# Optimization experiments

Hardware: AMD Instinct MI355X
Metric: run time of the kernel (lower is better)

Reference implementation:

```python
import jax, jax.numpy as jnp
import numpy as np

B, S, D = 4, 2048, 1024
H = 3 * D  # MLP hidden


def setup_inputs() -> dict:
    key = jax.random.key(0)
    ks = jax.random.split(key, 12)
    s = 1.0 / np.sqrt(D)
    n = lambda k, shape, sc: (jax.random.normal(k, shape, jnp.float32) * sc)
    return {
        "x": n(ks[0], (B, S, D), 1.0),
        "ln1_g": jnp.ones((D,), jnp.float32), "ln1_b": jnp.zeros((D,), jnp.float32),
        "ln2_g": jnp.ones((D,), jnp.float32), "ln2_b": jnp.zeros((D,), jnp.float32),
        "Wq": n(ks[1], (D, D), s), "bq": jnp.zeros((D,), jnp.float32),
        "Wk": n(ks[2], (D, D), s), "bk": jnp.zeros((D,), jnp.float32),
        "Wv": n(ks[3], (D, D), s), "bv": jnp.zeros((D,), jnp.float32),
        "Wi": n(ks[4], (D, 1), s), "bi": jnp.zeros((1,), jnp.float32),
        "Wf": n(ks[5], (D, 1), s), "bf": jnp.zeros((1,), jnp.float32),
        "Wo": n(ks[6], (D, D), s), "bo": jnp.zeros((D,), jnp.float32),
        "W1": n(ks[7], (D, H), s), "b1": jnp.zeros((H,), jnp.float32),
        "W2": n(ks[8], (H, D), 1.0 / np.sqrt(H)), "b2": jnp.zeros((D,), jnp.float32),
    }


def _layernorm(x, g, b, eps=1e-5):
    m = jnp.mean(x, axis=-1, keepdims=True)
    v = jnp.mean(jnp.square(x - m), axis=-1, keepdims=True)
    return (x - m) * jax.lax.rsqrt(v + eps) * g + b


def reference(x, ln1_g, ln1_b, ln2_g, ln2_b, Wq, bq, Wk, bk, Wv, bv,
              Wi, bi, Wf, bf, Wo, bo, W1, b1, W2, b2):
    seq = x.shape[1]
    h = _layernorm(x, ln1_g, ln1_b)
    # q, k computed in the original but unused in the score matrix (kept faithful)
    q = h @ Wq + bq
    k = h @ Wk + bk
    v = h @ Wv + bv                                  # [B,S,D]
    log_f = jax.nn.log_sigmoid(h @ Wf + bf)          # [B,S,1]
    log_i = jax.nn.log_sigmoid(h @ Wi + bi)          # [B,S,1]
    o = jax.nn.sigmoid(h @ Wo + bo)                  # [B,S,D]
    log_f_cum = jnp.cumsum(log_f, axis=1)            # [B,S,1]
    # log_scores[b,t,s] = log_i[b,s] + log_f_cum[b,t] - log_f_cum[b,s]
    log_scores = jnp.swapaxes(log_i, 1, 2) + log_f_cum - jnp.swapaxes(log_f_cum, 1, 2)
    causal = jnp.triu(jnp.full((seq, seq), -1e9, jnp.float32), k=1)
    scores = jnp.exp(log_scores + causal[None])      # [B,S,S]
    scores = scores / (jnp.sum(scores, axis=-1, keepdims=True) + 1e-6)
    attn = scores @ v                                # [B,S,D]
    x = x + o * attn
    h2 = _layernorm(x, ln2_g, ln2_b)
    m = h2 @ W1 + b1
    m = jnp.square(jnp.where(m > 0, m, 0.01 * m))    # LeakyReLU then square
    x = x + m @ W2 + b2
    return x
```

## Files before the change

kernel.cpp:

```cpp
#include <hip/hip_runtime.h>
#include <hip/hip_bf16.h>
#include <cstdint>

#define DI __device__ __forceinline__
typedef unsigned short u16;
using f32x4 = __attribute__((ext_vector_type(4))) float;
using bf16x8 = __attribute__((ext_vector_type(8))) short;

DI float bf16_bits_to_f32(u16 h) { return __uint_as_float(((unsigned int)h) << 16); }
DI u16 f32_to_bf16_bits(float f) {
    unsigned int u = __float_as_uint(f);
    unsigned int lsb = (u >> 16) & 1u;
    u += 0x7fffu + lsb;
    return (u16)(u >> 16);
}
DI float logsigf(float z) {
    if (z >= 0.f) return -log1pf(expf(-z));
    return z - log1pf(expf(z));
}
DI float lsef(float a, float b) {
    float mx = fmaxf(a, b), mn = fminf(a, b);
    return mx + log1pf(expf(mn - mx));
}
DI void ld4(float* d, const float* s) { *(float4*)d = *(const float4*)s; }

struct __align__(8) U4 { u16 a, b, c, d; };
union BF8 { u16 s[8]; uint4 v; };

DI void gload_lds16(const void* gsrc, void* ldst) {
    __builtin_amdgcn_global_load_lds(
        (const __attribute__((address_space(1))) uint32_t*)gsrc,
        (__attribute__((address_space(3))) uint32_t*)ldst,
        16, 0, 0);
}

__global__ void detect_kernel(const unsigned int* __restrict__ g1, int* __restrict__ flag) {
    if (threadIdx.x == 0 && blockIdx.x == 0)
        flag[0] = (g1[0] == 0x3F803F80u) ? 1 : 0;
}

struct SmallConv {
    const void* src[12];
    unsigned int dstOff[12];
    int n[12];
};
__global__ __launch_bounds__(256) void conv_small(
    SmallConv sc, float* __restrict__ wsf, const int* __restrict__ flag)
{
    const bool isbf = (flag[0] != 0);
    const int e = blockIdx.x;
    const void* s = sc.src[e];
    float* d = wsf + sc.dstOff[e];
    const int n = sc.n[e];
    for (int i = threadIdx.x; i < n; i += 256)
        d[i] = isbf ? bf16_bits_to_f32(((const u16*)s)[i]) : ((const float*)s)[i];
}

struct TransDesc {
    const void* src[4];
    unsigned int dstOff[4];
    int R[4], Cd[4];
    int start[5];
};
__global__ __launch_bounds__(256) void transpose_all(
    TransDesc td, u16* __restrict__ wsb, const int* __restrict__ flag)
{
    __shared__ float tile[64][65];
    const bool isbf = (flag[0] != 0);
    const int bid = blockIdx.x;
    int e = 0;
    if (bid >= td.start[1]) e = 1;
    if (bid >= td.start[2]) e = 2;
    if (bid >= td.start[3]) e = 3;
    const int local = bid - td.start[e];
    const int R = td.R[e], Cd = td.Cd[e];
    const int nbx = R >> 6;
    const int r0 = (local % nbx) * 64, c0 = (local / nbx) * 64;
    const void* src = td.src[e];
    u16* dst = wsb + td.dstOff[e];
    const int tid = threadIdx.x;
    #pragma unroll
    for (int i = 0; i < 16; ++i) {
        int idx = tid + i * 256;
        int lr = idx >> 6, lc = idx & 63;
        size_t g = (size_t)(r0 + lr) * Cd + c0 + lc;
        tile[lr][lc] = isbf ? bf16_bits_to_f32(((const u16*)src)[g]) : ((const float*)src)[g];
    }
    __syncthreads();
    #pragma unroll
    for (int i = 0; i < 16; ++i) {
        int idx = tid + i * 256;
        int lc2 = idx >> 6, lr2 = idx & 63;
        dst[(size_t)(c0 + lc2) * R + r0 + lr2] = f32_to_bf16_bits(tile[lr2][lc2]);
    }
}

DI float block_reduce_sum256(float v, float* sbuf) {
    #pragma unroll
    for (int off = 32; off > 0; off >>= 1) v += __shfl_down(v, off);
    int lane = threadIdx.x & 63, wid = threadIdx.x >> 6;
    if (lane == 0) sbuf[wid] = v;
    __syncthreads();
    float r = sbuf[0] + sbuf[1] + sbuf[2] + sbuf[3];
    __syncthreads();
    return r;
}

template<bool FI, bool RAW>
__global__ __launch_bounds__(256) void ln_kernel(
    const void* __restrict__ Xv, const int* __restrict__ flag,
    const float* __restrict__ gam, const float* __restrict__ bet,
    u16* __restrict__ Hout,
    const float* __restrict__ Wi, const float* __restrict__ bi,
    const float* __restrict__ Wf, const float* __restrict__ bf2,
    float* __restrict__ li, float* __restrict__ lf)
{
    __shared__ float sbuf[4];
    int row = blockIdx.x;
    int tid = threadIdx.x;
    size_t base = (size_t)row * 1024 + (size_t)tid * 4;
    float x[4];
    if (RAW && flag[0] != 0) {
        U4 u = *(const U4*)((const u16*)Xv + base);
        x[0] = bf16_bits_to_f32(u.a); x[1] = bf16_bits_to_f32(u.b);
        x[2] = bf16_bits_to_f32(u.c); x[3] = bf16_bits_to_f32(u.d);
    } else {
        ld4(x, (const float*)Xv + base);
    }
    float s = x[0] + x[1] + x[2] + x[3];
    s = block_reduce_sum256(s, sbuf);
    float mean = s * (1.f / 1024.f);
    float d[4], ss = 0.f;
    #pragma unroll
    for (int j = 0; j < 4; ++j) { d[j] = x[j] - mean; ss += d[j] * d[j]; }
    ss = block_reduce_sum256(ss, sbuf);
    float rstd = rsqrtf(ss * (1.f / 1024.f) + 1e-5f);
    float g4[4], b4[4];
    ld4(g4, gam + tid * 4); ld4(b4, bet + tid * 4);
    float h[4];
    #pragma unroll
    for (int j = 0; j < 4; ++j) h[j] = d[j] * rstd * g4[j] + b4[j];
    U4 hu;
    hu.a = f32_to_bf16_bits(h[0]); hu.b = f32_to_bf16_bits(h[1]);
    hu.c = f32_to_bf16_bits(h[2]); hu.d = f32_to_bf16_bits(h[3]);
    *(U4*)(Hout + base) = hu;
    if (FI) {
        float wi4[4], wf4[4];
        ld4(wi4, Wi + tid * 4); ld4(wf4, Wf + tid * 4);
        float pi = 0.f, pf = 0.f;
        #pragma unroll
        for (int j = 0; j < 4; ++j) { pi += h[j] * wi4[j]; pf += h[j] * wf4[j]; }
        pi = block_reduce_sum256(pi, sbuf);
        pf = block_reduce_sum256(pf, sbuf);
        if (tid == 0) {
            li[row] = logsigf(pi + bi[0]);
            lf[row] = logsigf(pf + bf2[0]);
        }
    }
}

__global__ __launch_bounds__(1024) void gates_kernel(
    const float* __restrict__ lf, const float* __restrict__ li,
    float* __restrict__ F, float* __restrict__ rsinv, int S)
{
    __shared__ float p[1024];
    __shared__ float q[1024];
    int b = blockIdx.x, t = threadIdx.x;
    float a = lf[b * S + 2 * t], c = lf[b * S + 2 * t + 1];
    float s2 = a + c;
    p[t] = s2; __syncthreads();
    #pragma unroll
    for (int off = 1; off < 1024; off <<= 1) {
        float add = (t >= off) ? p[t - off] : 0.f;
        __syncthreads();
        p[t] += add;
        __syncthreads();
    }
    float excl = p[t] - s2;
    float F0 = excl + a, F1 = excl + s2;
    F[b * S + 2 * t] = F0; F[b * S + 2 * t + 1] = F1;
    float g0 = li[b * S + 2 * t] - F0;
    float g1 = li[b * S + 2 * t + 1] - F1;
    float m2 = lsef(g0, g1);
    q[t] = m2; __syncthreads();
    #pragma unroll
    for (int off = 1; off < 1024; off <<= 1) {
        float add = (t >= off) ? q[t - off] : -1e30f;
        __syncthreads();
        float nv = lsef(q[t], add);
        __syncthreads();
        q[t] = nv;
        __syncthreads();
    }
    float lprev = (t > 0) ? q[t - 1] : -1e30f;
    float lc0 = lsef(lprev, g0);
    float lc1 = q[t];
    rsinv[b * S + 2 * t]     = 1.f / (expf(F0 + lc0) + 1e-6f);
    rsinv[b * S + 2 * t + 1] = 1.f / (expf(F1 + lc1) + 1e-6f);
}

__global__ __launch_bounds__(256) void wgen_kernel(
    const float* __restrict__ li, const float* __restrict__ F,
    const float* __restrict__ rsinv, u16* __restrict__ Wn)
{
    const int S = 2048;
    const int st = blockIdx.x, i = blockIdx.y, b = blockIdx.z;
    if (st >= 2 * i + 2) return;
    const int t0 = i * 128, s0 = st * 64;
    const int tid = threadIdx.x;
    const int lane = tid & 63, wave = tid >> 6;
    const int colb = (lane & 7) * 8;
    float lv[8], fv[8];
    ld4(lv, li + b * S + s0 + colb); ld4(lv + 4, li + b * S + s0 + colb + 4);
    ld4(fv, F + b * S + s0 + colb);  ld4(fv + 4, F + b * S + s0 + colb + 4);
    float g[8];
    #pragma unroll
    for (int j = 0; j < 8; ++j) g[j] = lv[j] - fv[j];
    #pragma unroll
    for (int r = 0; r < 4; ++r) {
        int row = wave * 32 + r * 8 + (lane >> 3);
        int t = t0 + row;
        float Ft = F[b * S + t];
        float ri = rsinv[b * S + t];
        BF8 wb;
        #pragma unroll
        for (int j = 0; j < 8; ++j) {
            int sg = s0 + colb + j;
            float w = (sg <= t) ? expf(g[j] + Ft) * ri : 0.f;
            wb.s[j] = f32_to_bf16_bits(w);
        }
        *(uint4*)(Wn + ((size_t)b * S + t) * S + s0 + colb) = wb.v;
    }
}

template<int EPI>
__global__ __launch_bounds__(256) void gemm_bt(
    const u16* __restrict__ A, const u16* __restrict__ Bt,
    const float* __restrict__ bias, u16* __restrict__ C,
    const float* __restrict__ resid, void* __restrict__ outp,
    const int* __restrict__ flag, int M, int N, int K)
{
    __shared__ short As[128 * 64];
    __shared__ short Bs[128 * 64];
    const int tid = threadIdx.x;
    const int lane = tid & 63;
    const int wave = tid >> 6;
    const int wm = wave >> 1, wn = wave & 1;
    const int m0 = blockIdx.x * 128, n0 = blockIdx.y * 128;

    const int srow = tid >> 3;
    const int sk = ((tid & 7) ^ (srow & 7)) * 8;
    const u16* aB = A  + (size_t)(m0 + srow) * K + sk;
    const u16* bB = Bt + (size_t)(n0 + srow) * K + sk;
    const size_t rowK32 = (size_t)32 * K;
    char* AsB = (char*)As + wave * 1024;
    char* BsB = (char*)Bs + wave * 1024;

    const int hi = lane >> 4;
    const int l7 = lane & 7;
    int ar[4], br[4];
    #pragma unroll
    for (int f = 0; f < 4; ++f) {
        ar[f] = (wm * 64 + f * 16 + (lane & 15)) * 64;
        br[f] = (wn * 64 + f * 16 + (lane & 15)) * 64;
    }

    f32x4 acc[4][4] = {};

    for (int k0 = 0; k0 < K; k0 += 64) {
        const u16* ga = aB; const u16* gb = bB;
        #pragma unroll
        for (int p = 0; p < 4; ++p) { gload_lds16(ga, AsB + p * 4096); ga += rowK32; }
        #pragma unroll
        for (int p = 0; p < 4; ++p) { gload_lds16(gb, BsB + p * 4096); gb += rowK32; }
        aB += 64; bB += 64;
        __syncthreads();
        #pragma unroll
        for (int kk = 0; kk < 2; ++kk) {
            const int co = ((kk * 4 + hi) ^ l7) * 8;
            bf16x8 af[4], bv[4];
            #pragma unroll
            for (int f = 0; f < 4; ++f) af[f] = *(const bf16x8*)&As[ar[f] + co];
            #pragma unroll
            for (int f = 0; f < 4; ++f) bv[f] = *(const bf16x8*)&Bs[br[f] + co];
            #pragma unroll
            for (int mf = 0; mf < 4; ++mf)
                #pragma unroll
                for (int nf = 0; nf < 4; ++nf)
                    acc[mf][nf] = __builtin_amdgcn_mfma_f32_16x16x32_bf16(
                        af[mf], bv[nf], acc[mf][nf], 0, 0, 0);
        }
        __syncthreads();
    }

    const bool outbf = (EPI == 3) ? (flag[0] != 0) : false;
    #pragma unroll
    for (int mf = 0; mf < 4; ++mf) {
        int r0 = m0 + wm * 64 + mf * 16 + (lane >> 4) * 4;
        #pragma unroll
        for (int nf = 0; nf < 4; ++nf) {
            int col = n0 + wn * 64 + nf * 16 + (lane & 15);
            float bsc = (EPI == 4) ? 0.f : bias[col];
            #pragma unroll
            for (int j = 0; j < 4; ++j) {
                int row = r0 + j;
                float v = acc[mf][nf][j] + ((EPI == 4) ? bias[row] : bsc);
                if constexpr (EPI == 4) {
                    C[(size_t)row * N + col] = f32_to_bf16_bits(v);
                } else if constexpr (EPI == 1) {
                    C[(size_t)row * N + col] = f32_to_bf16_bits(1.f / (1.f + expf(-v)));
                } else if constexpr (EPI == 2) {
                    float l = v > 0.f ? v : 0.01f * v;
                    C[(size_t)row * N + col] = f32_to_bf16_bits(l * l);
                } else {
                    size_t gi = (size_t)row * N + col;
                    v += resid[gi];
                    if (outbf) ((u16*)outp)[gi] = f32_to_bf16_bits(v);
                    else       ((float*)outp)[gi] = v;
                }
            }
        }
    }
}

__global__ __launch_bounds__(256) void attn_gemm(
    const u16* __restrict__ Wn, const u16* __restrict__ Vt,
    const u16* __restrict__ Ob, const void* __restrict__ Xraw,
    const int* __restrict__ flag, float* __restrict__ XF)
{
    const int S = 2048, D = 1024, NT = 8192;
    __shared__ short As[128 * 64];
    __shared__ short Bs[128 * 64];
    const int b  = blockIdx.z;
    const int it = 15 - blockIdx.x;
    const int t0 = it * 128;
    const int d0 = blockIdx.y * 128;
    const int tid = threadIdx.x;
    const int lane = tid & 63;
    const int wave = tid >> 6;
    const int wm = wave >> 1, wn = wave & 1;

    const int srow = tid >> 3;
    const int sk = ((tid & 7) ^ (srow & 7)) * 8;
    const u16* aB = Wn + ((size_t)b * S + t0 + srow) * S + sk;
    const u16* bB = Vt + (size_t)(d0 + srow) * NT + b * S + sk;
    char* AsB = (char*)As + wave * 1024;
    char* BsB = (char*)Bs + wave * 1024;

    const int hi = lane >> 4;
    const int l7 = lane & 7;
    int ar[4], br[4];
    #pragma unroll
    for (int f = 0; f < 4; ++f) {
        ar[f] = (wm * 64 + f * 16 + (lane & 15)) * 64;
        br[f] = (wn * 64 + f * 16 + (lane & 15)) * 64;
    }

    f32x4 acc[4][4] = {};
    const int nst = 2 * it + 2;
    for (int st = 0; st < nst; ++st) {
        const int s0 = st * 64;
        const u16* ga = aB + s0; const u16* gb = bB + s0;
        #pragma unroll
        for (int p = 0; p < 4; ++p) { gload_lds16(ga, AsB + p * 4096); ga += (size_t)32 * S; }
        #pragma unroll
        for (int p = 0; p < 4; ++p) { gload_lds16(gb, BsB + p * 4096); gb += (size_t)32 * NT; }
        __syncthreads();
        #pragma unroll
        for (int kk = 0; kk < 2; ++kk) {
            const int co = ((kk * 4 + hi) ^ l7) * 8;
            bf16x8 af[4], bv[4];
            #pragma unroll
            for (int f = 0; f < 4; ++f) af[f] = *(const bf16x8*)&As[ar[f] + co];
            #pragma unroll
            for (int f = 0; f < 4; ++f) bv[f] = *(const bf16x8*)&Bs[br[f] + co];
            #pragma unroll
            for (int mf = 0; mf < 4; ++mf)
                #pragma unroll
                for (int nf = 0; nf < 4; ++nf)
                    acc[mf][nf] = __builtin_amdgcn_mfma_f32_16x16x32_bf16(
                        af[mf], bv[nf], acc[mf][nf], 0, 0, 0);
        }
        __syncthreads();
    }

    const bool isbf = (flag[0] != 0);
    #pragma unroll
    for (int mf = 0; mf < 4; ++mf) {
        #pragma unroll
        for (int j = 0; j < 4; ++j) {
            int r = wm * 64 + mf * 16 + (lane >> 4) * 4 + j;
            int t = t0 + r;
            #pragma unroll
            for (int nf = 0; nf < 4; ++nf) {
                int dcol = d0 + wn * 64 + nf * 16 + (lane & 15);
                size_t base = ((size_t)b * S + t) * D + dcol;
                float o = bf16_bits_to_f32(Ob[base]);
                float xv = isbf ? bf16_bits_to_f32(((const u16*)Xraw)[base])
                                : ((const float*)Xraw)[base];
                XF[base] = xv + o * acc[mf][nf][j];
            }
        }
    }
}

static constexpr size_t OFB_LI   = 4096;
static constexpr size_t OFB_LF   = 36864;
static constexpr size_t OFB_F    = 69632;
static constexpr size_t OFB_G1   = 102400;
static constexpr size_t OFB_B1LN = 106496;
static constexpr size_t OFB_G2   = 110592;
static constexpr size_t OFB_B2LN = 114688;
static constexpr size_t OFB_BV   = 118784;
static constexpr size_t OFB_BO   = 122880;
static constexpr size_t OFB_WI   = 126976;
static constexpr size_t OFB_WF   = 131072;
static constexpr size_t OFB_B1   = 135168;
static constexpr size_t OFB_B2B  = 147456;
static constexpr size_t OFB_BI   = 151552;
static constexpr size_t OFB_BF   = 152576;
static constexpr size_t OFB_RS   = 200704;
static constexpr size_t OFB_XF   = 1048576;
static constexpr size_t OFB_H    = OFB_XF + 33554432;
static constexpr size_t OFB_V    = OFB_H + 16777216;
static constexpr size_t OFB_O    = OFB_V + 16777216;
static constexpr size_t OFB_M    = OFB_O + 16777216;
static constexpr size_t OFB_WVT  = OFB_M + 50331648;
static constexpr size_t OFB_WOT  = OFB_WVT + 2097152;
static constexpr size_t OFB_W1T  = OFB_WOT + 2097152;
static constexpr size_t OFB_W2T  = OFB_W1T + 6291456;
static constexpr size_t WS_BYTES = OFB_W2T + 6291456;

extern "C" void kernel_launch(void* const* d_in, const int* in_sizes, int n_in,
                              void* d_out, int out_size, void* d_ws, size_t ws_size,
                              hipStream_t stream) {
    (void)in_sizes; (void)n_in; (void)out_size;
    if (ws_size < WS_BYTES) return;
    char* ws = (char*)d_ws;
    int* flag = (int*)ws;
    auto FP = [&](size_t off) { return (float*)(ws + off); };
    auto HP = [&](size_t off) { return (u16*)(ws + off); };

    detect_kernel<<<1, 64, 0, stream>>>((const unsigned int*)d_in[1], flag);

    SmallConv sc;
    const int   srcIdx[12] = {1, 2, 3, 4, 10, 16, 11, 12, 13, 14, 18, 20};
    const size_t dstOff[12] = {OFB_G1, OFB_B1LN, OFB_G2, OFB_B2LN, OFB_BV, OFB_BO,
                               OFB_WI, OFB_BI, OFB_WF, OFB_BF, OFB_B1, OFB_B2B};
    const int   cnt[12] = {1024, 1024, 1024, 1024, 1024, 1024, 1024, 1, 1024, 1, 3072, 1024};
    for (int e = 0; e < 12; ++e) {
        sc.src[e] = d_in[srcIdx[e]];
        sc.dstOff[e] = (unsigned int)(dstOff[e] / 4);
        sc.n[e] = cnt[e];
    }
    conv_small<<<12, 256, 0, stream>>>(sc, (float*)ws, flag);

    TransDesc td;
    td.src[0] = d_in[9];  td.dstOff[0] = (unsigned int)(OFB_WVT / 2); td.R[0] = 1024; td.Cd[0] = 1024;
    td.src[1] = d_in[15]; td.dstOff[1] = (unsigned int)(OFB_WOT / 2); td.R[1] = 1024; td.Cd[1] = 1024;
    td.src[2] = d_in[17]; td.dstOff[2] = (unsigned int)(OFB_W1T / 2); td.R[2] = 1024; td.Cd[2] = 3072;
    td.src[3] = d_in[19]; td.dstOff[3] = (unsigned int)(OFB_W2T / 2); td.R[3] = 3072; td.Cd[3] = 1024;
    td.start[0] = 0; td.start[1] = 256; td.start[2] = 512; td.start[3] = 1280; td.start[4] = 2048;
    transpose_all<<<2048, 256, 0, stream>>>(td, (u16*)ws, flag);

    ln_kernel<true, true><<<8192, 256, 0, stream>>>(
        d_in[0], flag, FP(OFB_G1), FP(OFB_B1LN), HP(OFB_H),
        FP(OFB_WI), FP(OFB_BI), FP(OFB_WF), FP(OFB_BF),
        FP(OFB_LI), FP(OFB_LF));

    gates_kernel<<<4, 1024, 0, stream>>>(FP(OFB_LF), FP(OFB_LI), FP(OFB_F), FP(OFB_RS), 2048);

    wgen_kernel<<<dim3(32, 16, 4), 256, 0, stream>>>(
        FP(OFB_LI), FP(OFB_F), FP(OFB_RS), HP(OFB_M));

    gemm_bt<4><<<dim3(8, 64), 256, 0, stream>>>(
        HP(OFB_WVT), HP(OFB_H), FP(OFB_BV), HP(OFB_V),
        nullptr, nullptr, flag, 1024, 8192, 1024);
    gemm_bt<1><<<dim3(64, 8), 256, 0, stream>>>(
        HP(OFB_H), HP(OFB_WOT), FP(OFB_BO), HP(OFB_O),
        nullptr, nullptr, flag, 8192, 1024, 1024);

    attn_gemm<<<dim3(16, 8, 4), 256, 0, stream>>>(
        HP(OFB_M), HP(OFB_V), HP(OFB_O), d_in[0], flag, FP(OFB_XF));

    ln_kernel<false, false><<<8192, 256, 0, stream>>>(
        FP(OFB_XF), flag, FP(OFB_G2), FP(OFB_B2LN), HP(OFB_H),
        nullptr, nullptr, nullptr, nullptr, nullptr, nullptr);

    gemm_bt<2><<<dim3(64, 24), 256, 0, stream>>>(
        HP(OFB_H), HP(OFB_W1T), FP(OFB_B1), HP(OFB_M),
        nullptr, nullptr, flag, 8192, 3072, 1024);
    gemm_bt<3><<<dim3(64, 8), 256, 0, stream>>>(
        HP(OFB_M), HP(OFB_W2T), FP(OFB_B2B), nullptr,
        FP(OFB_XF), d_out, flag, 8192, 1024, 3072);
}
```

Before: 323.0 us.

## Merge prep kernels, fuse V/O GEMMs, and add XCD-aware block swizzle

Drops the dtype-detect kernel by having each kernel check the gamma word inline, and merges the small-parameter conversion and the weight transpose into one prep launch. The V and O projections now run in a single launch along grid z. An 8-way block-index swizzle is added to the generic GEMM, the fused V/O GEMM and the attention GEMM so neighbouring tiles land on the same chiplet for better L2 reuse. The aim is fewer launches and better cache locality, at the cost of a branchy fused kernel and a swizzle that assumes the block count divides by 8.

New measurement: 349.8 us. 8.3% more time.

```diff
diff --git a/kernel.cpp b/kernel.cpp
--- a/kernel.cpp
+++ b/kernel.cpp
@@ -23,6 +23,7 @@
     return mx + log1pf(expf(mn - mx));
 }
 DI void ld4(float* d, const float* s) { *(float4*)d = *(const float4*)s; }
+DI bool is_bf16(const unsigned int* g1w) { return g1w[0] == 0x3F803F80u; }
 
 struct __align__(8) U4 { u16 a, b, c, d; };
 union BF8 { u16 s[8]; uint4 v; };
@@ -34,50 +35,40 @@
         16, 0, 0);
 }
 
-__global__ void detect_kernel(const unsigned int* __restrict__ g1, int* __restrict__ flag) {
-    if (threadIdx.x == 0 && blockIdx.x == 0)
-        flag[0] = (g1[0] == 0x3F803F80u) ? 1 : 0;
-}
-
-struct SmallConv {
-    const void* src[12];
-    unsigned int dstOff[12];
-    int n[12];
+struct PrepDesc {
+    const void* csrc[12];
+    unsigned int cdst[12];
+    int cn[12];
+    const void* tsrc[4];
+    unsigned int tdst[4];
+    int tR[4], tCd[4];
+    int tstart[5];
 };
-__global__ __launch_bounds__(256) void conv_small(
-    SmallConv sc, float* __restrict__ wsf, const int* __restrict__ flag)
-{
-    const bool isbf = (flag[0] != 0);
-    const int e = blockIdx.x;
-    const void* s = sc.src[e];
-    float* d = wsf + sc.dstOff[e];
-    const int n = sc.n[e];
-    for (int i = threadIdx.x; i < n; i += 256)
-        d[i] = isbf ? bf16_bits_to_f32(((const u16*)s)[i]) : ((const float*)s)[i];
-}
-
-struct TransDesc {
-    const void* src[4];
-    unsigned int dstOff[4];
-    int R[4], Cd[4];
-    int start[5];
-};
-__global__ __launch_bounds__(256) void transpose_all(
-    TransDesc td, u16* __restrict__ wsb, const int* __restrict__ flag)
-{
+__global__ __launch_bounds__(256) void prep_kernel(
+    PrepDesc pd, char* __restrict__ ws, const unsigned int* __restrict__ g1w)
+{
+    const bool isbf = is_bf16(g1w);
+    const int bid = blockIdx.x;
+    if (bid < 12) {
+        const void* s = pd.csrc[bid];
+        float* d = (float*)ws + pd.cdst[bid];
+        const int n = pd.cn[bid];
+        for (int i = threadIdx.x; i < n; i += 256)
+            d[i] = isbf ? bf16_bits_to_f32(((const u16*)s)[i]) : ((const float*)s)[i];
+        return;
+    }
     __shared__ float tile[64][65];
-    const bool isbf = (flag[0] != 0);
-    const int bid = blockIdx.x;
+    const int b2 = bid - 12;
     int e = 0;
-    if (bid >= td.start[1]) e = 1;
-    if (bid >= td.start[2]) e = 2;
-    if (bid >= td.start[3]) e = 3;
-    const int local = bid - td.start[e];
-    const int R = td.R[e], Cd = td.Cd[e];
+    if (b2 >= pd.tstart[1]) e = 1;
+    if (b2 >= pd.tstart[2]) e = 2;
+    if (b2 >= pd.tstart[3]) e = 3;
+    const int local = b2 - pd.tstart[e];
+    const int R = pd.tR[e], Cd = pd.tCd[e];
     const int nbx = R >> 6;
     const int r0 = (local % nbx) * 64, c0 = (local / nbx) * 64;
-    const void* src = td.src[e];
-    u16* dst = wsb + td.dstOff[e];
+    const void* src = pd.tsrc[e];
+    u16* dst = (u16*)ws + pd.tdst[e];
     const int tid = threadIdx.x;
     #pragma unroll
     for (int i = 0; i < 16; ++i) {
@@ -108,7 +99,7 @@
 
 template<bool FI, bool RAW>
 __global__ __launch_bounds__(256) void ln_kernel(
-    const void* __restrict__ Xv, const int* __restrict__ flag,
+    const void* __restrict__ Xv, const unsigned int* __restrict__ g1w,
     const float* __restrict__ gam, const float* __restrict__ bet,
     u16* __restrict__ Hout,
     const float* __restrict__ Wi, const float* __restrict__ bi,
@@ -120,7 +111,7 @@
     int tid = threadIdx.x;
     size_t base = (size_t)row * 1024 + (size_t)tid * 4;
     float x[4];
-    if (RAW && flag[0] != 0) {
+    if (RAW && is_bf16(g1w)) {
         U4 u = *(const U4*)((const u16*)Xv + base);
         x[0] = bf16_bits_to_f32(u.a); x[1] = bf16_bits_to_f32(u.b);
         x[2] = bf16_bits_to_f32(u.c); x[3] = bf16_bits_to_f32(u.d);
@@ -238,7 +229,7 @@
     const u16* __restrict__ A, const u16* __restrict__ Bt,
     const float* __restrict__ bias, u16* __restrict__ C,
     const float* __restrict__ resid, void* __restrict__ outp,
-    const int* __restrict__ flag, int M, int N, int K)
+    const unsigned int* __restrict__ g1w, int M, int N, int K)
 {
     __shared__ short As[128 * 64];
     __shared__ short Bs[128 * 64];
@@ -246,7 +237,12 @@
     const int lane = tid & 63;
     const int wave = tid >> 6;
     const int wm = wave >> 1, wn = wave & 1;
-    const int m0 = blockIdx.x * 128, n0 = blockIdx.y * 128;
+
+    const int nwg = gridDim.x * gridDim.y;
+    const int flat = blockIdx.y * gridDim.x + blockIdx.x;
+    const int swz = (flat & 7) * (nwg >> 3) + (flat >> 3);
+    const int m0 = (swz % gridDim.x) * 128;
+    const int n0 = (swz / gridDim.x) * 128;
 
     const int srow = tid >> 3;
     const int sk = ((tid & 7) ^ (srow & 7)) * 8;
@@ -293,23 +289,19 @@
         __syncthreads();
     }
 
-    const bool outbf = (EPI == 3) ? (flag[0] != 0) : false;
+    const bool outbf = (EPI == 3) ? is_bf16(g1w) : false;
     #pragma unroll
     for (int mf = 0; mf < 4; ++mf) {
         int r0 = m0 + wm * 64 + mf * 16 + (lane >> 4) * 4;
         #pragma unroll
         for (int nf = 0; nf < 4; ++nf) {
             int col = n0 + wn * 64 + nf * 16 + (lane & 15);
-            float bsc = (EPI == 4) ? 0.f : bias[col];
+            float bsc = bias[col];
             #pragma unroll
             for (int j = 0; j < 4; ++j) {
                 int row = r0 + j;
-                float v = acc[mf][nf][j] + ((EPI == 4) ? bias[row] : bsc);
-                if constexpr (EPI == 4) {
-                    C[(size_t)row * N + col] = f32_to_bf16_bits(v);
-                } else if constexpr (EPI == 1) {
-                    C[(size_t)row * N + col] = f32_to_bf16_bits(1.f / (1.f + expf(-v)));
-                } else if constexpr (EPI == 2) {
+                float v = acc[mf][nf][j] + bsc;
+                if constexpr (EPI == 2) {
                     float l = v > 0.f ? v : 0.01f * v;
                     C[(size_t)row * N + col] = f32_to_bf16_bits(l * l);
                 } else {
@@ -323,18 +315,109 @@
     }
 }
 
+__global__ __launch_bounds__(256) void gemm_vo(
+    const u16* __restrict__ H, const u16* __restrict__ WOT, const u16* __restrict__ WVT,
+    const float* __restrict__ bo, const float* __restrict__ bv,
+    u16* __restrict__ O, u16* __restrict__ V)
+{
+    __shared__ short As[128 * 64];
+    __shared__ short Bs[128 * 64];
+    const int tid = threadIdx.x;
+    const int lane = tid & 63;
+    const int wave = tid >> 6;
+    const int wm = wave >> 1, wn = wave & 1;
+    const int K = 1024;
+
+    const int z = blockIdx.z;
+    const int flat = blockIdx.y * 64 + blockIdx.x;
+    const int swz = (flat & 7) * 64 + (flat >> 3);
+    const int sx = swz % 64, sy = swz / 64;
+    const u16* A;  const u16* Bt; int m0, n0, N;
+    u16* C;
+    if (z == 0) { A = H;   Bt = WOT; m0 = sx * 128; n0 = sy * 128; N = 1024; C = O; }
+    else        { A = WVT; Bt = H;   m0 = sy * 128; n0 = sx * 128; N = 8192; C = V; }
+
+    const int srow = tid >> 3;
+    const int sk = ((tid & 7) ^ (srow & 7)) * 8;
+    const u16* aB = A  + (size_t)(m0 + srow) * K + sk;
+    const u16* bB = Bt + (size_t)(n0 + srow) * K + sk;
+    const size_t rowK32 = (size_t)32 * K;
+    char* AsB = (char*)As + wave * 1024;
+    char* BsB = (char*)Bs + wave * 1024;
+
+    const int hi = lane >> 4;
+    const int l7 = lane & 7;
+    int ar[4], br[4];
+    #pragma unroll
+    for (int f = 0; f < 4; ++f) {
+        ar[f] = (wm * 64 + f * 16 + (lane & 15)) * 64;
+        br[f] = (wn * 64 + f * 16 + (lane & 15)) * 64;
+    }
+
+    f32x4 acc[4][4] = {};
+
+    for (int k0 = 0; k0 < K; k0 += 64) {
+        const u16* ga = aB; const u16* gb = bB;
+        #pragma unroll
+        for (int p = 0; p < 4; ++p) { gload_lds16(ga, AsB + p * 4096); ga += rowK32; }
+        #pragma unroll
+        for (int p = 0; p < 4; ++p) { gload_lds16(gb, BsB + p * 4096); gb += rowK32; }
+        aB += 64; bB += 64;
+        __syncthreads();
+        #pragma unroll
+        for (int kk = 0; kk < 2; ++kk) {
+            const int co = ((kk * 4 + hi) ^ l7) * 8;
+            bf16x8 af[4], bv4[4];
+            #pragma unroll
+            for (int f = 0; f < 4; ++f) af[f] = *(const bf16x8*)&As[ar[f] + co];
+            #pragma unroll
+            for (int f = 0; f < 4; ++f) bv4[f] = *(const bf16x8*)&Bs[br[f] + co];
+            #pragma unroll
+            for (int mf = 0; mf < 4; ++mf)
+                #pragma unroll
+                for (int nf = 0; nf < 4; ++nf)
+                    acc[mf][nf] = __builtin_amdgcn_mfma_f32_16x16x32_bf16(
+                        af[mf], bv4[nf], acc[mf][nf], 0, 0, 0);
+        }
+        __syncthreads();
+    }
+
+    #pragma unroll
+    for (int mf = 0; mf < 4; ++mf) {
+        int r0 = m0 + wm * 64 + mf * 16 + (lane >> 4) * 4;
+        #pragma unroll
+        for (int nf = 0; nf < 4; ++nf) {
+            int col = n0 + wn * 64 + nf * 16 + (lane & 15);
+            #pragma unroll
+            for (int j = 0; j < 4; ++j) {
+                int row = r0 + j;
+                float v;
+                if (z == 0) {
+                    v = acc[mf][nf][j] + bo[col];
+                    v = 1.f / (1.f + expf(-v));
+                } else {
+                    v = acc[mf][nf][j] + bv[row];
+                }
+                C[(size_t)row * N + col] = f32_to_bf16_bits(v);
+            }
+        }
+    }
+}
+
 __global__ __launch_bounds__(256) void attn_gemm(
     const u16* __restrict__ Wn, const u16* __restrict__ Vt,
     const u16* __restrict__ Ob, const void* __restrict__ Xraw,
-    const int* __restrict__ flag, float* __restrict__ XF)
+    const unsigned int* __restrict__ g1w, float* __restrict__ XF)
 {
     const int S = 2048, D = 1024, NT = 8192;
     __shared__ short As[128 * 64];
     __shared__ short Bs[128 * 64];
     const int b  = blockIdx.z;
-    const int it = 15 - blockIdx.x;
+    const int flat = blockIdx.y * 16 + blockIdx.x;
+    const int swz = (flat & 7) * 16 + (flat >> 3);
+    const int it = 15 - (swz % 16);
     const int t0 = it * 128;
-    const int d0 = blockIdx.y * 128;
+    const int d0 = (swz / 16) * 128;
     const int tid = threadIdx.x;
     const int lane = tid & 63;
     const int wave = tid >> 6;
@@ -384,7 +467,7 @@
         __syncthreads();
     }
 
-    const bool isbf = (flag[0] != 0);
+    const bool isbf = is_bf16(g1w);
     #pragma unroll
     for (int mf = 0; mf < 4; ++mf) {
         #pragma unroll
@@ -437,34 +520,29 @@
     (void)in_sizes; (void)n_in; (void)out_size;
     if (ws_size < WS_BYTES) return;
     char* ws = (char*)d_ws;
-    int* flag = (int*)ws;
+    const unsigned int* g1w = (const unsigned int*)d_in[1];
     auto FP = [&](size_t off) { return (float*)(ws + off); };
     auto HP = [&](size_t off) { return (u16*)(ws + off); };
 
-    detect_kernel<<<1, 64, 0, stream>>>((const unsigned int*)d_in[1], flag);
-
-    SmallConv sc;
+    PrepDesc pd;
     const int   srcIdx[12] = {1, 2, 3, 4, 10, 16, 11, 12, 13, 14, 18, 20};
     const size_t dstOff[12] = {OFB_G1, OFB_B1LN, OFB_G2, OFB_B2LN, OFB_BV, OFB_BO,
                                OFB_WI, OFB_BI, OFB_WF, OFB_BF, OFB_B1, OFB_B2B};
     const int   cnt[12] = {1024, 1024, 1024, 1024, 1024, 1024, 1024, 1, 1024, 1, 3072, 1024};
     for (int e = 0; e < 12; ++e) {
-        sc.src[e] = d_in[srcIdx[e]];
-        sc.dstOff[e] = (unsigned int)(dstOff[e] / 4);
-        sc.n[e] = cnt[e];
-    }
-    conv_small<<<12, 256, 0, stream>>>(sc, (float*)ws, flag);
-
-    TransDesc td;
-    td.src[0] = d_in[9];  td.dstOff[0] = (unsigned int)(OFB_WVT / 2); td.R[0] = 1024; td.Cd[0] = 1024;
-    td.src[1] = d_in[15]; td.dstOff[1] = (unsigned int)(OFB_WOT / 2); td.R[1] = 1024; td.Cd[1] = 1024;
-    td.src[2] = d_in[17]; td.dstOff[2] = (unsigned int)(OFB_W1T / 2); td.R[2] = 1024; td.Cd[2] = 3072;
-    td.src[3] = d_in[19]; td.dstOff[3] = (unsigned int)(OFB_W2T / 2); td.R[3] = 3072; td.Cd[3] = 1024;
-    td.start[0] = 0; td.start[1] = 256; td.start[2] = 512; td.start[3] = 1280; td.start[4] = 2048;
-    transpose_all<<<2048, 256, 0, stream>>>(td, (u16*)ws, flag);
+        pd.csrc[e] = d_in[srcIdx[e]];
+        pd.cdst[e] = (unsigned int)(dstOff[e] / 4);
+        pd.cn[e] = cnt[e];
+    }
+    pd.tsrc[0] = d_in[9];  pd.tdst[0] = (unsigned int)(OFB_WVT / 2); pd.tR[0] = 1024; pd.tCd[0] = 1024;
+    pd.tsrc[1] = d_in[15]; pd.tdst[1] = (unsigned int)(OFB_WOT / 2); pd.tR[1] = 1024; pd.tCd[1] = 1024;
+    pd.tsrc[2] = d_in[17]; pd.tdst[2] = (unsigned int)(OFB_W1T / 2); pd.tR[2] = 1024; pd.tCd[2] = 3072;
+    pd.tsrc[3] = d_in[19]; pd.tdst[3] = (unsigned int)(OFB_W2T / 2); pd.tR[3] = 3072; pd.tCd[3] = 1024;
+    pd.tstart[0] = 0; pd.tstart[1] = 256; pd.tstart[2] = 512; pd.tstart[3] = 1280; pd.tstart[4] = 2048;
+    prep_kernel<<<2060, 256, 0, stream>>>(pd, ws, g1w);
 
     ln_kernel<true, true><<<8192, 256, 0, stream>>>(
-        d_in[0], flag, FP(OFB_G1), FP(OFB_B1LN), HP(OFB_H),
+        d_in[0], g1w, FP(OFB_G1), FP(OFB_B1LN), HP(OFB_H),
         FP(OFB_WI), FP(OFB_BI), FP(OFB_WF), FP(OFB_BF),
         FP(OFB_LI), FP(OFB_LF));
 
@@ -473,24 +551,21 @@
     wgen_kernel<<<dim3(32, 16, 4), 256, 0, stream>>>(
         FP(OFB_LI), FP(OFB_F), FP(OFB_RS), HP(OFB_M));
 
-    gemm_bt<4><<<dim3(8, 64), 256, 0, stream>>>(
-        HP(OFB_WVT), HP(OFB_H), FP(OFB_BV), HP(OFB_V),
-        nullptr, nullptr, flag, 1024, 8192, 1024);
-    gemm_bt<1><<<dim3(64, 8), 256, 0, stream>>>(
-        HP(OFB_H), HP(OFB_WOT), FP(OFB_BO), HP(OFB_O),
-        nullptr, nullptr, flag, 8192, 1024, 1024);
+    gemm_vo<<<dim3(64, 8, 2), 256, 0, stream>>>(
+        HP(OFB_H), HP(OFB_WOT), HP(OFB_WVT), FP(OFB_BO), FP(OFB_BV),
+        HP(OFB_O), HP(OFB_V));
 
     attn_gemm<<<dim3(16, 8, 4), 256, 0, stream>>>(
-        HP(OFB_M), HP(OFB_V), HP(OFB_O), d_in[0], flag, FP(OFB_XF));
+        HP(OFB_M), HP(OFB_V), HP(OFB_O), d_in[0], g1w, FP(OFB_XF));
 
     ln_kernel<false, false><<<8192, 256, 0, stream>>>(
-        FP(OFB_XF), flag, FP(OFB_G2), FP(OFB_B2LN), HP(OFB_H),
+        FP(OFB_XF), g1w, FP(OFB_G2), FP(OFB_B2LN), HP(OFB_H),
         nullptr, nullptr, nullptr, nullptr, nullptr, nullptr);
 
     gemm_bt<2><<<dim3(64, 24), 256, 0, stream>>>(
         HP(OFB_H), HP(OFB_W1T), FP(OFB_B1), HP(OFB_M),
-        nullptr, nullptr, flag, 8192, 3072, 1024);
+        nullptr, nullptr, g1w, 8192, 3072, 1024);
     gemm_bt<3><<<dim3(64, 8), 256, 0, stream>>>(
         HP(OFB_M), HP(OFB_W2T), FP(OFB_B2B), nullptr,
-        FP(OFB_XF), d_out, flag, 8192, 1024, 3072);
-}
+        FP(OFB_XF), d_out, g1w, 8192, 1024, 3072);
+}
```
